# Performance work log

Hardware: AMD Instinct MI355X
Metric: run time of the kernel (lower is better)

## Reference

```python
import jax, jax.numpy as jnp
import numpy as np

B, T, D = 64, 2048, 512
UNITS = 512


def setup_inputs() -> dict:
    key = jax.random.key(0)
    ks = jax.random.split(key, 8)
    s = 1.0 / np.sqrt(D)
    return {
        "decoder_hidden": jax.random.normal(ks[0], (B, D), dtype=jnp.float32),
        "encoder_output": jax.random.normal(ks[1], (B, T, D), dtype=jnp.float32),
        "W1": jax.random.normal(ks[2], (D, UNITS), dtype=jnp.float32) * s,
        "b1": jnp.zeros((UNITS,), dtype=jnp.float32),
        "W2": jax.random.normal(ks[3], (D, UNITS), dtype=jnp.float32) * s,
        "b2": jnp.zeros((UNITS,), dtype=jnp.float32),
        "V": jax.random.normal(ks[4], (UNITS, 1), dtype=jnp.float32) * (1.0 / np.sqrt(UNITS)),
        "bV": jnp.zeros((1,), dtype=jnp.float32),
    }


def reference(decoder_hidden, encoder_output, W1, b1, W2, b2, V, bV):
    # query projection: [B, 1, U]
    q = (decoder_hidden @ W1 + b1)[:, None, :]
    # key projection: [B, T, U]
    k = jnp.einsum('btd,du->btu', encoder_output, W2) + b2
    score = jnp.tanh(q + k)                       # [B, T, U]
    logits = score @ V + bV                       # [B, T, 1]
    attention_weights = jax.nn.softmax(logits, axis=1)  # [B, T, 1]
    context_vector = jnp.sum(attention_weights * encoder_output, axis=1)  # [B, D]
    return context_vector, attention_weights
```

## Files before the change

kernel.cpp:

```cpp
#include <hip/hip_runtime.h>
#include <stdint.h>

constexpr int NB = 64;
constexpr int NT = 2048;
constexpr int ND = 512;
constexpr int NU = 512;

typedef float f32x4 __attribute__((ext_vector_type(4)));
typedef float f32x16 __attribute__((ext_vector_type(16)));
typedef short bf16x8 __attribute__((ext_vector_type(8)));

__device__ __forceinline__ unsigned short f2bf(float x) {
  union { float f; unsigned int u; } v; v.f = x;
  unsigned int r = v.u + 0x7FFFu + ((v.u >> 16) & 1u);
  return (unsigned short)(r >> 16);
}

__device__ __forceinline__ float fast_tanh(float x) {
  return 1.0f - 2.0f / (__expf(2.0f * x) + 1.0f);
}

__global__ __launch_bounds__(512) void qproj_kernel(
    const float* __restrict__ dh, const float* __restrict__ W1,
    const float* __restrict__ b1, const float* __restrict__ b2,
    float* __restrict__ q) {
  int b = blockIdx.x;
  int u = threadIdx.x;
  const float* dr = dh + b * ND;
  float a0 = 0.f, a1 = 0.f, a2 = 0.f, a3 = 0.f;
  for (int k = 0; k < ND; k += 4) {
    a0 = fmaf(dr[k + 0], W1[(size_t)(k + 0) * NU + u], a0);
    a1 = fmaf(dr[k + 1], W1[(size_t)(k + 1) * NU + u], a1);
    a2 = fmaf(dr[k + 2], W1[(size_t)(k + 2) * NU + u], a2);
    a3 = fmaf(dr[k + 3], W1[(size_t)(k + 3) * NU + u], a3);
  }
  q[b * NU + u] = b1[u] + b2[u] + ((a0 + a1) + (a2 + a3));
}

__global__ __launch_bounds__(256) void packW2_kernel(
    const float* __restrict__ W2, unsigned short* __restrict__ w2p) {
  int tid = blockIdx.x * 256 + threadIdx.x;
  int lane = tid & 63;
  int ntg = (tid >> 6) & 15;
  int ks = tid >> 10;
  int col = ntg * 32 + (lane & 31);
  int k0 = ks * 16 + ((lane >> 5) << 3);
  const float* src = W2 + (size_t)k0 * NU + col;
  ushort4 lo, hi;
  lo.x = f2bf(src[0 * NU]); lo.y = f2bf(src[1 * NU]);
  lo.z = f2bf(src[2 * NU]); lo.w = f2bf(src[3 * NU]);
  hi.x = f2bf(src[4 * NU]); hi.y = f2bf(src[5 * NU]);
  hi.z = f2bf(src[6 * NU]); hi.w = f2bf(src[7 * NU]);
  ushort4* dst = (ushort4*)(w2p + (size_t)tid * 8);
  dst[0] = lo; dst[1] = hi;
}

__global__ __launch_bounds__(512, 4) void logits_kernel(
    const float* __restrict__ enc, const unsigned short* __restrict__ w2p,
    const float* __restrict__ q, const float* __restrict__ Vw,
    float* __restrict__ logits) {
  __shared__ unsigned short encA[64 * 512];
  __shared__ float red[8][64];

  const int tid = threadIdx.x;
  const int wave = tid >> 6;
  const int lane = tid & 63;
  const int wg = blockIdx.x;
  const int b = wg >> 5;
  const int tch = wg & 31;

  const char* bbase = (const char*)w2p + (size_t)(((2 * wave) * 64 + lane)) * 16;

  bf16x8 b0a = *(const bf16x8*)(bbase);
  bf16x8 b0b = *(const bf16x8*)(bbase + 1024);
  bf16x8 b1a = *(const bf16x8*)(bbase + 16384);
  bf16x8 b1b = *(const bf16x8*)(bbase + 16384 + 1024);

  const float4* encBase = (const float4*)(enc + ((size_t)b * NT + (size_t)tch * 64) * ND);
#pragma unroll 4
  for (int i = 0; i < 8; ++i) {
    int idx8 = i * 512 + tid;
    int row = idx8 >> 6;
    int c8 = idx8 & 63;
    float4 v0 = encBase[idx8 * 2];
    float4 v1 = encBase[idx8 * 2 + 1];
    unsigned int p0, p1, p2, p3;
    asm("v_cvt_pk_bf16_f32 %0, %1, %2" : "=v"(p0) : "v"(v0.x), "v"(v0.y));
    asm("v_cvt_pk_bf16_f32 %0, %1, %2" : "=v"(p1) : "v"(v0.z), "v"(v0.w));
    asm("v_cvt_pk_bf16_f32 %0, %1, %2" : "=v"(p2) : "v"(v1.x), "v"(v1.y));
    asm("v_cvt_pk_bf16_f32 %0, %1, %2" : "=v"(p3) : "v"(v1.z), "v"(v1.w));
    uint4 pk; pk.x = p0; pk.y = p1; pk.z = p2; pk.w = p3;
    int byteoff = row * 1024 + ((c8 * 16) ^ ((row & 7) << 4));
    *(uint4*)((char*)encA + byteoff) = pk;
  }

  f32x16 acc00 = {}, acc01 = {}, acc10 = {}, acc11 = {};

  const int arow0 = (lane & 31) * 1024;
  const int arow1 = arow0 + 32 * 1024;
  const int aswz = ((lane & 31) & 7) << 4;
  const int kfix = (lane >> 5) << 4;

  __syncthreads();

#pragma unroll
  for (int ks = 0; ks < 32; ks += 2) {
    int ka = (ks * 32 + kfix) ^ aswz;
    bf16x8 a0 = *(const bf16x8*)((const char*)encA + arow0 + ka);
    bf16x8 a1 = *(const bf16x8*)((const char*)encA + arow1 + ka);
    __builtin_amdgcn_s_setprio(1);
    acc00 = __builtin_amdgcn_mfma_f32_32x32x16_bf16(a0, b0a, acc00, 0, 0, 0);
    acc01 = __builtin_amdgcn_mfma_f32_32x32x16_bf16(a0, b0b, acc01, 0, 0, 0);
    acc10 = __builtin_amdgcn_mfma_f32_32x32x16_bf16(a1, b0a, acc10, 0, 0, 0);
    acc11 = __builtin_amdgcn_mfma_f32_32x32x16_bf16(a1, b0b, acc11, 0, 0, 0);
    __builtin_amdgcn_s_setprio(0);
    if (ks + 2 < 32) {
      b0a = *(const bf16x8*)(bbase + (ks + 2) * 16384);
      b0b = *(const bf16x8*)(bbase + (ks + 2) * 16384 + 1024);
    }
    int kb = ((ks + 1) * 32 + kfix) ^ aswz;
    bf16x8 a2 = *(const bf16x8*)((const char*)encA + arow0 + kb);
    bf16x8 a3 = *(const bf16x8*)((const char*)encA + arow1 + kb);
    __builtin_amdgcn_s_setprio(1);
    acc00 = __builtin_amdgcn_mfma_f32_32x32x16_bf16(a2, b1a, acc00, 0, 0, 0);
    acc01 = __builtin_amdgcn_mfma_f32_32x32x16_bf16(a2, b1b, acc01, 0, 0, 0);
    acc10 = __builtin_amdgcn_mfma_f32_32x32x16_bf16(a3, b1a, acc10, 0, 0, 0);
    acc11 = __builtin_amdgcn_mfma_f32_32x32x16_bf16(a3, b1b, acc11, 0, 0, 0);
    __builtin_amdgcn_s_setprio(0);
    if (ks + 3 < 32) {
      b1a = *(const bf16x8*)(bbase + (ks + 3) * 16384);
      b1b = *(const bf16x8*)(bbase + (ks + 3) * 16384 + 1024);
    }
  }

  const int col = lane & 31;
  const float qv0 = q[b * NU + wave * 64 + col];
  const float qv1 = q[b * NU + wave * 64 + 32 + col];
  const float Vv0 = Vw[wave * 64 + col];
  const float Vv1 = Vw[wave * 64 + 32 + col];
  const int hi4 = (lane >> 5) << 2;

#pragma unroll
  for (int amt = 0; amt < 2; ++amt) {
#pragma unroll
    for (int reg = 0; reg < 16; ++reg) {
      float c0 = amt ? acc10[reg] : acc00[reg];
      float c1 = amt ? acc11[reg] : acc01[reg];
      float s = fast_tanh(c0 + qv0) * Vv0 + fast_tanh(c1 + qv1) * Vv1;
      s += __shfl_xor(s, 1);
      s += __shfl_xor(s, 2);
      s += __shfl_xor(s, 4);
      s += __shfl_xor(s, 8);
      s += __shfl_xor(s, 16);
      if (col == 0) {
        int row = (reg & 3) + ((reg >> 2) << 3) + hi4;
        red[wave][amt * 32 + row] = s;
      }
    }
  }
  __syncthreads();
  if (tid < 64) {
    float t = 0.f;
#pragma unroll
    for (int w = 0; w < 8; ++w) t += red[w][tid];
    logits[(size_t)b * NT + (size_t)tch * 64 + tid] = t;
  }
}

__global__ __launch_bounds__(512) void softmax_kernel(float* __restrict__ wts) {
  int b = blockIdx.x;
  int tid = threadIdx.x;
  float4* base = (float4*)(wts + (size_t)b * NT);
  float4 v = base[tid];
  float m = fmaxf(fmaxf(v.x, v.y), fmaxf(v.z, v.w));
#pragma unroll
  for (int d = 1; d < 64; d <<= 1) m = fmaxf(m, __shfl_xor(m, d));
  __shared__ float sm[8];
  __shared__ float ss[8];
  int w = tid >> 6;
  if ((tid & 63) == 0) sm[w] = m;
  __syncthreads();
  float M = sm[0];
#pragma unroll
  for (int i = 1; i < 8; ++i) M = fmaxf(M, sm[i]);
  float e0 = __expf(v.x - M), e1 = __expf(v.y - M), e2 = __expf(v.z - M), e3 = __expf(v.w - M);
  float s = e0 + e1 + e2 + e3;
#pragma unroll
  for (int d = 1; d < 64; d <<= 1) s += __shfl_xor(s, d);
  if ((tid & 63) == 0) ss[w] = s;
  __syncthreads();
  float S = 0.f;
#pragma unroll
  for (int i = 0; i < 8; ++i) S += ss[i];
  float inv = 1.0f / S;
  base[tid] = (float4){e0 * inv, e1 * inv, e2 * inv, e3 * inv};
}

__global__ __launch_bounds__(512) void ctx_partial_kernel(
    const float* __restrict__ enc, const float* __restrict__ wts,
    float* __restrict__ partials) {
  int bx = blockIdx.x;
  int b = bx >> 4;
  int slice = bx & 15;
  int tid = threadIdx.x;
  const float* e = enc + ((size_t)b * NT + (size_t)slice * 128) * ND + tid;
  const float* wp = wts + (size_t)b * NT + slice * 128;
  float acc = 0.0f;
#pragma unroll 4
  for (int tt = 0; tt < 128; ++tt) {
    acc = fmaf(wp[tt], e[(size_t)tt * ND], acc);
  }
  partials[(size_t)bx * ND + tid] = acc;
}

__global__ __launch_bounds__(512) void ctx_combine_kernel(
    const float* __restrict__ partials, float* __restrict__ ctx) {
  int b = blockIdx.x;
  int tid = threadIdx.x;
  float s = 0.0f;
#pragma unroll
  for (int i = 0; i < 16; ++i) s += partials[((size_t)b * 16 + i) * ND + tid];
  ctx[(size_t)b * ND + tid] = s;
}

extern "C" void kernel_launch(void* const* d_in, const int* in_sizes, int n_in,
                              void* d_out, int out_size, void* d_ws, size_t ws_size,
                              hipStream_t stream) {
  const float* dh  = (const float*)d_in[0];
  const float* enc = (const float*)d_in[1];
  const float* W1  = (const float*)d_in[2];
  const float* b1  = (const float*)d_in[3];
  const float* W2  = (const float*)d_in[4];
  const float* b2  = (const float*)d_in[5];
  const float* Vw  = (const float*)d_in[6];

  float* q            = (float*)d_ws;
  unsigned short* w2p = (unsigned short*)((char*)d_ws + 131072);
  float* partials     = (float*)((char*)d_ws + 655360);

  float* ctx = (float*)d_out;
  float* wts = (float*)d_out + NB * ND;

  qproj_kernel<<<NB, 512, 0, stream>>>(dh, W1, b1, b2, q);
  packW2_kernel<<<128, 256, 0, stream>>>(W2, w2p);
  logits_kernel<<<NB * (NT / 64), 512, 0, stream>>>(enc, w2p, q, Vw, wts);
  softmax_kernel<<<NB, 512, 0, stream>>>(wts);
  ctx_partial_kernel<<<NB * 16, 512, 0, stream>>>(enc, wts, partials);
  ctx_combine_kernel<<<NB, 512, 0, stream>>>(partials, ctx);
}
```

Measured before the change: 181.4 us.

## Transpose logits GEMM so W2 is the A operand and reduce along registers

The MFMA operands are swapped so the weight tiles sit in the A slot and the encoder tile stored in LDS is the B operand. The encoder tile is written in a new XOR-swizzled, K-major LDS layout, and four weight register sets are kept in flight to prefetch deeper. Because the unit dimension now runs along accumulator registers, the tanh-times-V reduction is mostly in-register with one cross-half shuffle, replacing the per-element 5-step shuffle tree. q and V are staged in LDS and read as float4. In exchange the kernel uses more registers and a little more LDS, which may lower occupancy, and it depends on the new swizzle being both correct and free of bank conflicts.

```diff
diff --git a/kernel.cpp b/kernel.cpp
--- a/kernel.cpp
+++ b/kernel.cpp
@@ -59,7 +59,8 @@
     const float* __restrict__ enc, const unsigned short* __restrict__ w2p,
     const float* __restrict__ q, const float* __restrict__ Vw,
     float* __restrict__ logits) {
-  __shared__ unsigned short encA[64 * 512];
+  __shared__ unsigned short encB[64 * 512];
+  __shared__ float qV[2][NU];
   __shared__ float red[8][64];
 
   const int tid = threadIdx.x;
@@ -68,20 +69,33 @@
   const int wg = blockIdx.x;
   const int b = wg >> 5;
   const int tch = wg & 31;
-
-  const char* bbase = (const char*)w2p + (size_t)(((2 * wave) * 64 + lane)) * 16;
-
-  bf16x8 b0a = *(const bf16x8*)(bbase);
-  bf16x8 b0b = *(const bf16x8*)(bbase + 1024);
-  bf16x8 b1a = *(const bf16x8*)(bbase + 16384);
-  bf16x8 b1b = *(const bf16x8*)(bbase + 16384 + 1024);
+  const char* w2pc = (const char*)w2p;
+
+  const int bsub = ((2 * wave) * 64 + lane) * 16;
+  int voff = bsub;
+  bf16x8 a0a = *(const bf16x8*)(w2pc + voff);
+  bf16x8 a0b = *(const bf16x8*)(w2pc + voff + 1024);
+  voff += 16384;
+  bf16x8 a1a = *(const bf16x8*)(w2pc + voff);
+  bf16x8 a1b = *(const bf16x8*)(w2pc + voff + 1024);
+  voff += 16384;
+  bf16x8 a2a = *(const bf16x8*)(w2pc + voff);
+  bf16x8 a2b = *(const bf16x8*)(w2pc + voff + 1024);
+  voff += 16384;
+  bf16x8 a3a = *(const bf16x8*)(w2pc + voff);
+  bf16x8 a3b = *(const bf16x8*)(w2pc + voff + 1024);
+  voff += 16384;
+
+  qV[0][tid] = q[b * NU + tid];
+  qV[1][tid] = Vw[tid];
 
   const float4* encBase = (const float4*)(enc + ((size_t)b * NT + (size_t)tch * 64) * ND);
-#pragma unroll 4
+  char* eB = (char*)encB;
+#pragma unroll
   for (int i = 0; i < 8; ++i) {
     int idx8 = i * 512 + tid;
-    int row = idx8 >> 6;
-    int c8 = idx8 & 63;
+    int t = idx8 >> 6;
+    int kc = idx8 & 63;
     float4 v0 = encBase[idx8 * 2];
     float4 v1 = encBase[idx8 * 2 + 1];
     unsigned int p0, p1, p2, p3;
@@ -90,80 +104,75 @@
     asm("v_cvt_pk_bf16_f32 %0, %1, %2" : "=v"(p2) : "v"(v1.x), "v"(v1.y));
     asm("v_cvt_pk_bf16_f32 %0, %1, %2" : "=v"(p3) : "v"(v1.z), "v"(v1.w));
     uint4 pk; pk.x = p0; pk.y = p1; pk.z = p2; pk.w = p3;
-    int byteoff = row * 1024 + ((c8 * 16) ^ ((row & 7) << 4));
-    *(uint4*)((char*)encA + byteoff) = pk;
+    int waddr = kc * 1024 + (((t ^ kc) & 63) << 4);
+    *(uint4*)(eB + waddr) = pk;
   }
 
   f32x16 acc00 = {}, acc01 = {}, acc10 = {}, acc11 = {};
 
-  const int arow0 = (lane & 31) * 1024;
-  const int arow1 = arow0 + 32 * 1024;
-  const int aswz = ((lane & 31) & 7) << 4;
-  const int kfix = (lane >> 5) << 4;
-
-  __syncthreads();
-
-#pragma unroll
-  for (int ks = 0; ks < 32; ks += 2) {
-    int ka = (ks * 32 + kfix) ^ aswz;
-    bf16x8 a0 = *(const bf16x8*)((const char*)encA + arow0 + ka);
-    bf16x8 a1 = *(const bf16x8*)((const char*)encA + arow1 + ka);
-    __builtin_amdgcn_s_setprio(1);
-    acc00 = __builtin_amdgcn_mfma_f32_32x32x16_bf16(a0, b0a, acc00, 0, 0, 0);
-    acc01 = __builtin_amdgcn_mfma_f32_32x32x16_bf16(a0, b0b, acc01, 0, 0, 0);
-    acc10 = __builtin_amdgcn_mfma_f32_32x32x16_bf16(a1, b0a, acc10, 0, 0, 0);
-    acc11 = __builtin_amdgcn_mfma_f32_32x32x16_bf16(a1, b0b, acc11, 0, 0, 0);
-    __builtin_amdgcn_s_setprio(0);
-    if (ks + 2 < 32) {
-      b0a = *(const bf16x8*)(bbase + (ks + 2) * 16384);
-      b0b = *(const bf16x8*)(bbase + (ks + 2) * 16384 + 1024);
-    }
-    int kb = ((ks + 1) * 32 + kfix) ^ aswz;
-    bf16x8 a2 = *(const bf16x8*)((const char*)encA + arow0 + kb);
-    bf16x8 a3 = *(const bf16x8*)((const char*)encA + arow1 + kb);
-    __builtin_amdgcn_s_setprio(1);
-    acc00 = __builtin_amdgcn_mfma_f32_32x32x16_bf16(a2, b1a, acc00, 0, 0, 0);
-    acc01 = __builtin_amdgcn_mfma_f32_32x32x16_bf16(a2, b1b, acc01, 0, 0, 0);
-    acc10 = __builtin_amdgcn_mfma_f32_32x32x16_bf16(a3, b1a, acc10, 0, 0, 0);
-    acc11 = __builtin_amdgcn_mfma_f32_32x32x16_bf16(a3, b1b, acc11, 0, 0, 0);
-    __builtin_amdgcn_s_setprio(0);
-    if (ks + 3 < 32) {
-      b1a = *(const bf16x8*)(bbase + (ks + 3) * 16384);
-      b1b = *(const bf16x8*)(bbase + (ks + 3) * 16384 + 1024);
-    }
-  }
-
-  const int col = lane & 31;
-  const float qv0 = q[b * NU + wave * 64 + col];
-  const float qv1 = q[b * NU + wave * 64 + 32 + col];
-  const float Vv0 = Vw[wave * 64 + col];
-  const float Vv1 = Vw[wave * 64 + 32 + col];
-  const int hi4 = (lane >> 5) << 2;
-
-#pragma unroll
-  for (int amt = 0; amt < 2; ++amt) {
-#pragma unroll
-    for (int reg = 0; reg < 16; ++reg) {
-      float c0 = amt ? acc10[reg] : acc00[reg];
-      float c1 = amt ? acc11[reg] : acc01[reg];
-      float s = fast_tanh(c0 + qv0) * Vv0 + fast_tanh(c1 + qv1) * Vv1;
-      s += __shfl_xor(s, 1);
-      s += __shfl_xor(s, 2);
-      s += __shfl_xor(s, 4);
-      s += __shfl_xor(s, 8);
-      s += __shfl_xor(s, 16);
-      if (col == 0) {
-        int row = (reg & 3) + ((reg >> 2) << 3) + hi4;
-        red[wave][amt * 32 + row] = s;
-      }
-    }
+  const int hi = lane >> 5;
+  const int Lb0 = (hi * 1040) ^ ((lane & 31) << 4);
+  const int Lb1 = (hi * 1040) ^ (((lane & 31) + 32) << 4);
+
+  __syncthreads();
+
+#define PHASE(I, AA, AB)                                                           \
+  {                                                                                \
+    bf16x8 e0 = *(const bf16x8*)(eB + (Lb0 ^ ((I) * 2080)));                       \
+    bf16x8 e1 = *(const bf16x8*)(eB + (Lb1 ^ ((I) * 2080)));                       \
+    __builtin_amdgcn_s_setprio(1);                                                 \
+    acc00 = __builtin_amdgcn_mfma_f32_32x32x16_bf16(AA, e0, acc00, 0, 0, 0);       \
+    acc01 = __builtin_amdgcn_mfma_f32_32x32x16_bf16(AA, e1, acc01, 0, 0, 0);       \
+    acc10 = __builtin_amdgcn_mfma_f32_32x32x16_bf16(AB, e0, acc10, 0, 0, 0);       \
+    acc11 = __builtin_amdgcn_mfma_f32_32x32x16_bf16(AB, e1, acc11, 0, 0, 0);       \
+    __builtin_amdgcn_s_setprio(0);                                                 \
+    AA = *(const bf16x8*)(w2pc + voff);                                            \
+    AB = *(const bf16x8*)(w2pc + voff + 1024);                                     \
+    voff += 16384;                                                                 \
+  }
+#pragma unroll
+  for (int i = 0; i < 32; i += 4) {
+    PHASE(i + 0, a0a, a0b)
+    PHASE(i + 1, a1a, a1b)
+    PHASE(i + 2, a2a, a2b)
+    PHASE(i + 3, a3a, a3b)
+  }
+#undef PHASE
+
+  const int hi4 = hi << 2;
+  float s0 = 0.f, s1 = 0.f;
+#pragma unroll
+  for (int rg = 0; rg < 4; ++rg) {
+    int uo = wave * 64 + 8 * rg + hi4;
+    float4 qq = *(const float4*)&qV[0][uo];
+    float4 vv = *(const float4*)&qV[1][uo];
+    s0 += fast_tanh(acc00[4 * rg + 0] + qq.x) * vv.x + fast_tanh(acc00[4 * rg + 1] + qq.y) * vv.y
+        + fast_tanh(acc00[4 * rg + 2] + qq.z) * vv.z + fast_tanh(acc00[4 * rg + 3] + qq.w) * vv.w;
+    s1 += fast_tanh(acc01[4 * rg + 0] + qq.x) * vv.x + fast_tanh(acc01[4 * rg + 1] + qq.y) * vv.y
+        + fast_tanh(acc01[4 * rg + 2] + qq.z) * vv.z + fast_tanh(acc01[4 * rg + 3] + qq.w) * vv.w;
+  }
+#pragma unroll
+  for (int rg = 0; rg < 4; ++rg) {
+    int uo = wave * 64 + 32 + 8 * rg + hi4;
+    float4 qq = *(const float4*)&qV[0][uo];
+    float4 vv = *(const float4*)&qV[1][uo];
+    s0 += fast_tanh(acc10[4 * rg + 0] + qq.x) * vv.x + fast_tanh(acc10[4 * rg + 1] + qq.y) * vv.y
+        + fast_tanh(acc10[4 * rg + 2] + qq.z) * vv.z + fast_tanh(acc10[4 * rg + 3] + qq.w) * vv.w;
+    s1 += fast_tanh(acc11[4 * rg + 0] + qq.x) * vv.x + fast_tanh(acc11[4 * rg + 1] + qq.y) * vv.y
+        + fast_tanh(acc11[4 * rg + 2] + qq.z) * vv.z + fast_tanh(acc11[4 * rg + 3] + qq.w) * vv.w;
+  }
+  s0 += __shfl_xor(s0, 32);
+  s1 += __shfl_xor(s1, 32);
+  if (lane < 32) {
+    red[wave][lane] = s0;
+    red[wave][32 + lane] = s1;
   }
   __syncthreads();
   if (tid < 64) {
-    float t = 0.f;
-#pragma unroll
-    for (int w = 0; w < 8; ++w) t += red[w][tid];
-    logits[(size_t)b * NT + (size_t)tch * 64 + tid] = t;
+    float s = 0.f;
+#pragma unroll
+    for (int w = 0; w < 8; ++w) s += red[w][tid];
+    logits[(size_t)b * NT + (size_t)tch * 64 + tid] = s;
   }
 }
 
```

Measured after the change: 460.3 us. 2.54x slower.
